# Kernel optimization log

Hardware: AMD Instinct MI355X
Metric: run time of the kernel (lower is better)

Reference implementation:

```python
import jax, jax.numpy as jnp
import numpy as np

EMBED_DIM = 1024
HIDDEN = 4 * EMBED_DIM
BATCH, SEQ = 4, 4096
EPS = 1e-5


def setup_inputs() -> dict:
    key = jax.random.key(0)
    k1, k2, k3 = jax.random.split(key, 3)
    x = jax.random.normal(k1, (BATCH, SEQ, EMBED_DIM), dtype=jnp.float32)
    # Kaiming-ish init scale for linear weights
    w1 = jax.random.normal(k2, (HIDDEN, EMBED_DIM), dtype=jnp.float32) * (1.0 / np.sqrt(EMBED_DIM))
    w2 = jax.random.normal(k3, (EMBED_DIM, HIDDEN), dtype=jnp.float32) * (1.0 / np.sqrt(HIDDEN))
    return {"x": x, "w1": w1, "w2": w2}


def _quant_weight(w):
    # BitNet-b1.58 absmean ternary quantization: clip(round(w/s), -1, 1) * s
    s = jnp.clip(jnp.mean(jnp.abs(w)), EPS, None)
    wq = jnp.clip(jnp.round(w / s), -1.0, 1.0) * s
    # straight-through estimator
    return w + jax.lax.stop_gradient(wq - w)


def _quant_act(x):
    # int8 per-token absmax quantization of activations
    scale = 127.0 / jnp.clip(jnp.max(jnp.abs(x), axis=-1, keepdims=True), EPS, None)
    xq = jnp.clip(jnp.round(x * scale), -128.0, 127.0) / scale
    return x + jax.lax.stop_gradient(xq - x)


def _bitlinear(x, w):
    # x: [..., in], w: [out, in] -> [..., out]
    return jnp.einsum('bsi,oi->bso', _quant_act(x), _quant_weight(w))


def reference(x, w1, w2):
    h = jax.nn.gelu(_bitlinear(x, w1), approximate=False)  # nn.GELU default = exact erf
    return _bitlinear(h, w2)  # dropout is identity in eval / p=0
```

## Files before the change

### kernel.cpp

```cpp
#include <hip/hip_runtime.h>
#include <hip/hip_bf16.h>
#include <cstdint>
#include <cmath>

typedef int intx4 __attribute__((ext_vector_type(4)));
typedef short shortx8 __attribute__((ext_vector_type(8)));

#define EPSQ 1e-5f

__device__ __forceinline__ void async16(const void* g, void* l) {
  __builtin_amdgcn_global_load_lds(
      (const __attribute__((address_space(1))) unsigned int*)(uintptr_t)g,
      (__attribute__((address_space(3))) unsigned int*)(unsigned int)(uintptr_t)l,
      16, 0, 0);
}

__device__ __forceinline__ int q8(float v, float scale, float lo, float hi) {
  return (int)fminf(fmaxf(rintf(v * scale), lo), hi);
}

__device__ __forceinline__ float fast_gelu(float y) {
  const float t = y * 0.70710678118654752f;
  const float x = fabsf(t);
  const float u = __builtin_amdgcn_rcpf(__builtin_fmaf(0.3275911f, x, 1.0f));
  float p = __builtin_fmaf(1.061405429f, u, -1.453152027f);
  p = __builtin_fmaf(p, u, 1.421413741f);
  p = __builtin_fmaf(p, u, -0.284496736f);
  p = __builtin_fmaf(p, u, 0.254829592f);
  p = p * u;
  const float e = __expf(-x * x);
  const float erf_abs = __builtin_fmaf(-p, e, 1.0f);
  const float erf_t = copysignf(erf_abs, t);
  return 0.5f * y * (1.0f + erf_t);
}

__global__ void k_init(float* rowmax, double* sums) {
  int i = blockIdx.x * 256 + threadIdx.x;
  if (i < 16384) rowmax[i] = 0.0f;
  if (i < 2) sums[i] = 0.0;
}

__global__ __launch_bounds__(256) void k_absmean2(const float* __restrict__ W1,
                                                  const float* __restrict__ W2,
                                                  double* __restrict__ sums) {
  __shared__ double wsum[4];
  const int tid = threadIdx.x;
  const int which = blockIdx.x >> 11;
  const float* __restrict__ W = which ? W2 : W1;
  const size_t base = ((size_t)(blockIdx.x & 2047) * 256 + tid) * 8;
  float4 a = *(const float4*)(W + base);
  float4 b = *(const float4*)(W + base + 4);
  float s = fabsf(a.x) + fabsf(a.y) + fabsf(a.z) + fabsf(a.w) +
            fabsf(b.x) + fabsf(b.y) + fabsf(b.z) + fabsf(b.w);
  double d = (double)s;
#pragma unroll
  for (int i = 1; i < 64; i <<= 1) d += __shfl_xor(d, i);
  const int lane = tid & 63, wave = tid >> 6;
  if (lane == 0) wsum[wave] = d;
  __syncthreads();
  if (tid == 0) atomicAdd(sums + which, wsum[0] + wsum[1] + wsum[2] + wsum[3]);
}

__global__ __launch_bounds__(256) void k_quantw2(const float* __restrict__ W1,
                                                 const float* __restrict__ W2,
                                                 signed char* __restrict__ W1Q,
                                                 signed char* __restrict__ W2Q,
                                                 const double* __restrict__ sums) {
  const int which = blockIdx.x >> 11;
  const float* __restrict__ W = which ? W2 : W1;
  signed char* __restrict__ WQ = which ? W2Q : W1Q;
  const float s = fmaxf((float)(sums[which] * (1.0 / 4194304.0)), EPSQ);
  const float inv_s = 1.0f / s;
  const size_t base = ((size_t)(blockIdx.x & 2047) * 256 + threadIdx.x) * 8;
  float4 a = *(const float4*)(W + base);
  float4 b = *(const float4*)(W + base + 4);
  float v[8] = {a.x, a.y, a.z, a.w, b.x, b.y, b.z, b.w};
  unsigned int lo = 0, hi = 0;
#pragma unroll
  for (int j = 0; j < 4; ++j) {
    lo |= ((unsigned int)(q8(v[j], inv_s, -1.f, 1.f) & 0xff)) << (8 * j);
    hi |= ((unsigned int)(q8(v[4 + j], inv_s, -1.f, 1.f) & 0xff)) << (8 * j);
  }
  uint2 o; o.x = lo; o.y = hi;
  *(uint2*)(WQ + base) = o;
}

__global__ __launch_bounds__(256) void k_quantx(const float* __restrict__ X,
                                                signed char* __restrict__ XQ,
                                                float* __restrict__ dqx) {
  __shared__ float wmax[4];
  const int row = blockIdx.x, tid = threadIdx.x;
  const size_t base = (size_t)row * 1024 + tid * 4;
  float4 a = *(const float4*)(X + base);
  float m = fmaxf(fmaxf(fabsf(a.x), fabsf(a.y)), fmaxf(fabsf(a.z), fabsf(a.w)));
#pragma unroll
  for (int i = 1; i < 64; i <<= 1) m = fmaxf(m, __shfl_xor(m, i));
  const int lane = tid & 63, wave = tid >> 6;
  if (lane == 0) wmax[wave] = m;
  __syncthreads();
  m = fmaxf(fmaxf(wmax[0], wmax[1]), fmaxf(wmax[2], wmax[3]));
  m = fmaxf(m, EPSQ);
  const float scale = 127.f / m;
  if (tid == 0) dqx[row] = m * (1.f / 127.f);
  unsigned int p = ((unsigned int)(q8(a.x, scale, -128.f, 127.f) & 0xff)) |
                   ((unsigned int)(q8(a.y, scale, -128.f, 127.f) & 0xff) << 8) |
                   ((unsigned int)(q8(a.z, scale, -128.f, 127.f) & 0xff) << 16) |
                   ((unsigned int)(q8(a.w, scale, -128.f, 127.f) & 0xff) << 24);
  *(unsigned int*)(XQ + base) = p;
}

template <int KB>
__device__ __forceinline__ void gemm_mainloop256(const signed char* __restrict__ A,
                                                 const signed char* __restrict__ B,
                                                 int bm, int bn, int tid, char* lds,
                                                 intx4 (&acc)[8][4]) {
  const int wave = tid >> 6, lane = tid & 63;
  const int wm = wave >> 2, wn = wave & 3;
  const int kq = lane >> 4, lc = lane & 15;
  constexpr int NT = KB / 64;

  size_t goff[4];
  int ldsbase[4];
#pragma unroll
  for (int i = 0; i < 4; ++i) {
    const int n = i * 512 + tid;
    const int m = n & 1023;
    const int r = m >> 2, g = m & 3;
    const int gl = g ^ ((r >> 1) & 3);
    const int rowbase = ((i < 2) ? bm : bn) * 256 + r;
    goff[i] = (size_t)rowbase * KB + gl * 16;
    ldsbase[i] = (i * 512 + wave * 64) * 16;
  }

  int aoff[8], boff[4];
#pragma unroll
  for (int mi = 0; mi < 8; ++mi) {
    const int r = wm * 128 + mi * 16 + lc;
    aoff[mi] = r * 64 + ((kq ^ ((r >> 1) & 3)) << 4);
  }
#pragma unroll
  for (int ni = 0; ni < 4; ++ni) {
    const int r = wn * 64 + ni * 16 + lc;
    boff[ni] = 16384 + r * 64 + ((kq ^ ((r >> 1) & 3)) << 4);
  }

#pragma unroll
  for (int mi = 0; mi < 8; ++mi)
#pragma unroll
    for (int ni = 0; ni < 4; ++ni) {
      intx4 z = {0, 0, 0, 0};
      acc[mi][ni] = z;
    }

#pragma unroll
  for (int t = 0; t < 3; ++t) {
    char* lslot = lds + (t & 3) * 32768;
    const size_t k0 = (size_t)t * 64;
#pragma unroll
    for (int i = 0; i < 4; ++i)
      async16(((i < 2) ? A : B) + goff[i] + k0, lslot + ldsbase[i]);
  }

  for (int t = 0; t < NT; ++t) {
    if (t + 2 < NT)      asm volatile("s_waitcnt vmcnt(8)" ::: "memory");
    else if (t + 1 < NT) asm volatile("s_waitcnt vmcnt(4)" ::: "memory");
    else                 asm volatile("s_waitcnt vmcnt(0)" ::: "memory");
    __builtin_amdgcn_s_barrier();
    __builtin_amdgcn_sched_barrier(0);
    if (t + 3 < NT) {
      char* lslot = lds + ((t + 3) & 3) * 32768;
      const size_t k0 = (size_t)(t + 3) * 64;
#pragma unroll
      for (int i = 0; i < 4; ++i)
        async16(((i < 2) ? A : B) + goff[i] + k0, lslot + ldsbase[i]);
    }
    char* lslot = lds + (t & 3) * 32768;
    intx4 af[8], bf[4];
#pragma unroll
    for (int mi = 0; mi < 8; ++mi) af[mi] = *(const intx4*)(lslot + aoff[mi]);
#pragma unroll
    for (int ni = 0; ni < 4; ++ni) bf[ni] = *(const intx4*)(lslot + boff[ni]);
    __builtin_amdgcn_s_setprio(1);
#pragma unroll
    for (int mi = 0; mi < 8; ++mi)
#pragma unroll
      for (int ni = 0; ni < 4; ++ni)
        acc[mi][ni] =
            __builtin_amdgcn_mfma_i32_16x16x64_i8(af[mi], bf[ni], acc[mi][ni], 0, 0, 0);
    __builtin_amdgcn_s_setprio(0);
  }
}

__global__ __launch_bounds__(512, 2) void k_gemm1(const signed char* __restrict__ A,
                                                  const signed char* __restrict__ B,
                                                  const float* __restrict__ dqx,
                                                  const double* __restrict__ sums,
                                                  short* __restrict__ HS,
                                                  float* __restrict__ mblk,
                                                  float* __restrict__ rowmax) {
  __shared__ __attribute__((aligned(16))) char lds[131072];
  const int tid = threadIdx.x;
  const int bm = blockIdx.x, bn = blockIdx.y;

  intx4 acc[8][4];
  gemm_mainloop256<1024>(A, B, bm, bn, tid, lds, acc);

  const int wave = tid >> 6, lane = tid & 63;
  const int wm = wave >> 2, wn = wave & 3;
  const int kq = lane >> 4, lc = lane & 15;
  const float s1 = fmaxf((float)(sums[0] * (1.0 / 4194304.0)), EPSQ);

  __syncthreads();
  float* smax = (float*)lds;
  if (tid < 256) smax[tid] = 0.0f;
  __syncthreads();

#pragma unroll
  for (int mi = 0; mi < 8; ++mi) {
#pragma unroll
    for (int r = 0; r < 4; ++r) {
      const int lrow = wm * 128 + mi * 16 + kq * 4 + r;
      const int crow = bm * 256 + lrow;
      const float f = s1 * dqx[crow];
      float mx = 0.f;
#pragma unroll
      for (int ni = 0; ni < 4; ++ni) {
        float y = (float)acc[mi][ni][r] * f;
        float h = fast_gelu(y);
        acc[mi][ni][r] = (int)__float_as_uint(h);
        mx = fmaxf(mx, fabsf(h));
      }
#pragma unroll
      for (int s = 1; s < 16; s <<= 1) mx = fmaxf(mx, __shfl_xor(mx, s));
      if (lc == 0) atomicMax((unsigned int*)&smax[lrow], __float_as_uint(mx));
    }
  }
  __syncthreads();
  if (tid < 256) {
    mblk[(size_t)(bm * 256 + tid) * 16 + bn] = smax[tid];
    atomicMax((unsigned int*)&rowmax[bm * 256 + tid], __float_as_uint(smax[tid]));
  }

#pragma unroll
  for (int mi = 0; mi < 8; ++mi) {
#pragma unroll
    for (int r = 0; r < 4; ++r) {
      const int lrow = wm * 128 + mi * 16 + kq * 4 + r;
      const int crow = bm * 256 + lrow;
      const float sc = 32767.0f / fmaxf(smax[lrow], 1e-30f);
#pragma unroll
      for (int ni = 0; ni < 4; ++ni) {
        const int gcol = bn * 256 + wn * 64 + ni * 16 + lc;
        float h = __uint_as_float((unsigned int)acc[mi][ni][r]);
        int v = (int)fminf(fmaxf(rintf(h * sc), -32767.f), 32767.f);
        HS[(size_t)crow * 4096 + gcol] = (short)v;
      }
    }
  }
}

__global__ __launch_bounds__(256) void k_quanth(const short* __restrict__ HS,
                                                const float* __restrict__ mblk,
                                                const float* __restrict__ rowmax,
                                                signed char* __restrict__ HQ) {
  const size_t gid = (size_t)blockIdx.x * 256 + threadIdx.x;
  const size_t base = gid * 8;
  const int row = (int)(base >> 12);
  const int blk = (int)((base >> 8) & 15);
  const float m = fmaxf(rowmax[row], EPSQ);
  const float fb = mblk[(size_t)row * 16 + blk] * (127.0f / 32767.0f) / m;
  shortx8 s = *(const shortx8*)(HS + base);
  unsigned int lo = 0, hi = 0;
#pragma unroll
  for (int j = 0; j < 4; ++j) {
    lo |= ((unsigned int)(q8((float)s[j], fb, -128.f, 127.f) & 0xff)) << (8 * j);
    hi |= ((unsigned int)(q8((float)s[4 + j], fb, -128.f, 127.f) & 0xff)) << (8 * j);
  }
  uint2 o; o.x = lo; o.y = hi;
  *(uint2*)(HQ + base) = o;
}

__global__ __launch_bounds__(512, 2) void k_gemm2(const signed char* __restrict__ A,
                                                  const signed char* __restrict__ B,
                                                  const float* __restrict__ rowmax,
                                                  const double* __restrict__ sums,
                                                  float* __restrict__ OUT) {
  __shared__ __attribute__((aligned(16))) char lds[131072];
  const int tid = threadIdx.x;
  const int bm = blockIdx.x, bn = blockIdx.y;

  intx4 acc[8][4];
  gemm_mainloop256<4096>(A, B, bm, bn, tid, lds, acc);

  const int wave = tid >> 6, lane = tid & 63;
  const int wm = wave >> 2, wn = wave & 3;
  const int kq = lane >> 4, lc = lane & 15;
  const float s2 = fmaxf((float)(sums[0] * (1.0 / 4194304.0)), EPSQ);
#pragma unroll
  for (int mi = 0; mi < 8; ++mi) {
#pragma unroll
    for (int r = 0; r < 4; ++r) {
      const int crow = bm * 256 + wm * 128 + mi * 16 + kq * 4 + r;
      const float dqh = fmaxf(rowmax[crow], EPSQ) * (1.f / 127.f);
      const float f = s2 * dqh;
#pragma unroll
      for (int ni = 0; ni < 4; ++ni) {
        const int gcol = bn * 256 + wn * 64 + ni * 16 + lc;
        OUT[(size_t)crow * 1024 + gcol] = (float)acc[mi][ni][r] * f;
      }
    }
  }
}

extern "C" void kernel_launch(void* const* d_in, const int* in_sizes, int n_in,
                              void* d_out, int out_size, void* d_ws, size_t ws_size,
                              hipStream_t stream) {
  const float* X  = (const float*)d_in[0];
  const float* W1 = (const float*)d_in[1];
  const float* W2 = (const float*)d_in[2];
  float* OUT = (float*)d_out;

  char* ws = (char*)d_ws;
  signed char* W1Q = (signed char*)(ws);
  signed char* W2Q = (signed char*)(ws + (4u << 20));
  float* DQX       = (float*)(ws + (8u << 20));
  float* ROWMAX    = (float*)(ws + (8u << 20) + 65536);
  double* SUMS     = (double*)(ws + (8u << 20) + 131072);
  float* MBLK      = (float*)(ws + (9u << 20));
  signed char* HQ  = (signed char*)(ws + (10u << 20));
  const size_t fixed = 74u << 20;
  short* HS = (short*)(ws + fixed);

  signed char* XQ = (signed char*)((char*)d_out + 50331648ull);

  int R = 256;
  const int cands[7] = {16384, 8192, 4096, 2048, 1024, 512, 256};
  for (int i = 0; i < 7; ++i) {
    if (fixed + (size_t)cands[i] * 8192ull <= ws_size) { R = cands[i]; break; }
  }

  hipLaunchKernelGGL(k_init, dim3(64), dim3(256), 0, stream, ROWMAX, SUMS);
  hipLaunchKernelGGL(k_absmean2, dim3(4096), dim3(256), 0, stream, W1, W2, SUMS);
  hipLaunchKernelGGL(k_quantw2, dim3(4096), dim3(256), 0, stream, W1, W2, W1Q, W2Q, SUMS);
  hipLaunchKernelGGL(k_quantx, dim3(16384), dim3(256), 0, stream, X, XQ, DQX);

  const int nchunk = 16384 / R;
  for (int c = 0; c < nchunk; ++c) {
    const int row0 = c * R;
    hipLaunchKernelGGL(k_gemm1, dim3(R / 256, 16), dim3(512), 0, stream,
                       XQ + (size_t)row0 * 1024, W1Q, DQX + row0, SUMS,
                       HS, MBLK + (size_t)row0 * 16, ROWMAX + row0);
    hipLaunchKernelGGL(k_quanth, dim3(R * 2), dim3(256), 0, stream,
                       HS, MBLK + (size_t)row0 * 16, ROWMAX + row0,
                       HQ + (size_t)row0 * 4096);
  }
  hipLaunchKernelGGL(k_gemm2, dim3(64, 4), dim3(512), 0, stream,
                     HQ, W2Q, ROWMAX, SUMS + 1, OUT);
}
```

Before: 418.5 us.

## Restructure GEMM mainloop to double-buffered K=128 stages, swizzle tiles, pack intermediate

The shared GEMM mainloop moves from a 4-slot K=64 async pipeline to a 2-slot K=128 double buffer with an XOR-swizzled LDS layout. The next-stage global loads are spread across four sub-phases that each end in a barrier, so loads overlap MFMA work. Both GEMMs now use a 1D grid with a block-index swizzle to improve L2 reuse. The gemm1 epilogue writes the int16 intermediate as vectorized 4-row packed words using v_cvt_pknorm_i16_f32, and k_quanth reads that packed layout, which adds layout complexity and slightly different rounding.

```diff
diff --git a/kernel.cpp b/kernel.cpp
--- a/kernel.cpp
+++ b/kernel.cpp
@@ -4,7 +4,6 @@
 #include <cmath>
 
 typedef int intx4 __attribute__((ext_vector_type(4)));
-typedef short shortx8 __attribute__((ext_vector_type(8)));
 
 #define EPSQ 1e-5f
 
@@ -17,6 +16,12 @@
 
 __device__ __forceinline__ int q8(float v, float scale, float lo, float hi) {
   return (int)fminf(fmaxf(rintf(v * scale), lo), hi);
+}
+
+__device__ __forceinline__ unsigned int pknorm_i16(float a, float b) {
+  unsigned int r;
+  asm("v_cvt_pknorm_i16_f32 %0, %1, %2" : "=v"(r) : "v"(a), "v"(b));
+  return r;
 }
 
 __device__ __forceinline__ float fast_gelu(float y) {
@@ -117,32 +122,20 @@
   const int wave = tid >> 6, lane = tid & 63;
   const int wm = wave >> 2, wn = wave & 3;
   const int kq = lane >> 4, lc = lane & 15;
-  constexpr int NT = KB / 64;
-
-  size_t goff[4];
-  int ldsbase[4];
-#pragma unroll
-  for (int i = 0; i < 4; ++i) {
-    const int n = i * 512 + tid;
-    const int m = n & 1023;
-    const int r = m >> 2, g = m & 3;
-    const int gl = g ^ ((r >> 1) & 3);
-    const int rowbase = ((i < 2) ? bm : bn) * 256 + r;
-    goff[i] = (size_t)rowbase * KB + gl * 16;
-    ldsbase[i] = (i * 512 + wave * 64) * 16;
-  }
-
-  int aoff[8], boff[4];
-#pragma unroll
-  for (int mi = 0; mi < 8; ++mi) {
-    const int r = wm * 128 + mi * 16 + lc;
-    aoff[mi] = r * 64 + ((kq ^ ((r >> 1) & 3)) << 4);
-  }
-#pragma unroll
-  for (int ni = 0; ni < 4; ++ni) {
-    const int r = wn * 64 + ni * 16 + lc;
-    boff[ni] = 16384 + r * 64 + ((kq ^ ((r >> 1) & 3)) << 4);
-  }
+  constexpr int NS = KB / 128;
+
+  const int rr = tid >> 3;
+  const int gs16 = (((tid & 7) ^ (rr & 7)) << 4);
+  unsigned int goff[8];
+#pragma unroll
+  for (int j = 0; j < 8; ++j) {
+    const int rowbase = ((j < 4) ? bm : bn) * 256 + (j & 3) * 64 + rr;
+    goff[j] = (unsigned int)rowbase * (unsigned int)KB + gs16;
+  }
+
+  const int fsw = ((kq ^ (lc & 7)) << 4);
+  const int abase = (wm * 128 + lc) * 128 + fsw;
+  const int bbase = 32768 + (wn * 64 + lc) * 128 + fsw;
 
 #pragma unroll
   for (int mi = 0; mi < 8; ++mi)
@@ -153,41 +146,66 @@
     }
 
 #pragma unroll
-  for (int t = 0; t < 3; ++t) {
-    char* lslot = lds + (t & 3) * 32768;
-    const size_t k0 = (size_t)t * 64;
-#pragma unroll
-    for (int i = 0; i < 4; ++i)
-      async16(((i < 2) ? A : B) + goff[i] + k0, lslot + ldsbase[i]);
-  }
-
-  for (int t = 0; t < NT; ++t) {
-    if (t + 2 < NT)      asm volatile("s_waitcnt vmcnt(8)" ::: "memory");
-    else if (t + 1 < NT) asm volatile("s_waitcnt vmcnt(4)" ::: "memory");
-    else                 asm volatile("s_waitcnt vmcnt(0)" ::: "memory");
-    __builtin_amdgcn_s_barrier();
-    __builtin_amdgcn_sched_barrier(0);
-    if (t + 3 < NT) {
-      char* lslot = lds + ((t + 3) & 3) * 32768;
-      const size_t k0 = (size_t)(t + 3) * 64;
-#pragma unroll
-      for (int i = 0; i < 4; ++i)
-        async16(((i < 2) ? A : B) + goff[i] + k0, lslot + ldsbase[i]);
+  for (int j = 0; j < 8; ++j)
+    async16(((j < 4) ? A : B) + (size_t)goff[j],
+            lds + j * 8192 + wave * 1024);
+  asm volatile("s_waitcnt vmcnt(0)" ::: "memory");
+  __builtin_amdgcn_s_barrier();
+  __builtin_amdgcn_sched_barrier(0);
+
+  for (int t = 0; t < NS; ++t) {
+    char* buf = lds + ((t & 1) << 16);
+    char* nbuf = lds + (((t + 1) & 1) << 16);
+    const size_t k0n = (size_t)(t + 1) * 128;
+    const bool more = (t + 1 < NS);
+    intx4 bf[4][2];
+#pragma unroll
+    for (int p = 0; p < 4; ++p) {
+      intx4 af[2][2];
+#pragma unroll
+      for (int h = 0; h < 2; ++h) {
+        const int o = abase + (2 * p + h) * 2048;
+        af[h][0] = *(const intx4*)(buf + o);
+        af[h][1] = *(const intx4*)(buf + (o ^ 64));
+      }
+      if (p == 0) {
+#pragma unroll
+        for (int ni = 0; ni < 4; ++ni) {
+          const int o = bbase + ni * 2048;
+          bf[ni][0] = *(const intx4*)(buf + o);
+          bf[ni][1] = *(const intx4*)(buf + (o ^ 64));
+        }
+      }
+      if (more) {
+        if (p == 0) {
+          async16(A + (size_t)goff[0] + k0n, nbuf + 0 * 8192 + wave * 1024);
+          async16(A + (size_t)goff[1] + k0n, nbuf + 1 * 8192 + wave * 1024);
+          async16(A + (size_t)goff[2] + k0n, nbuf + 2 * 8192 + wave * 1024);
+        } else if (p == 1) {
+          async16(A + (size_t)goff[3] + k0n, nbuf + 3 * 8192 + wave * 1024);
+          async16(B + (size_t)goff[4] + k0n, nbuf + 4 * 8192 + wave * 1024);
+          async16(B + (size_t)goff[5] + k0n, nbuf + 5 * 8192 + wave * 1024);
+        } else if (p == 2) {
+          async16(B + (size_t)goff[6] + k0n, nbuf + 6 * 8192 + wave * 1024);
+          async16(B + (size_t)goff[7] + k0n, nbuf + 7 * 8192 + wave * 1024);
+        }
+      }
+      __builtin_amdgcn_s_barrier();
+      __builtin_amdgcn_sched_barrier(0);
+      __builtin_amdgcn_s_setprio(1);
+#pragma unroll
+      for (int ks = 0; ks < 2; ++ks)
+#pragma unroll
+        for (int h = 0; h < 2; ++h)
+#pragma unroll
+          for (int ni = 0; ni < 4; ++ni)
+            acc[2 * p + h][ni] = __builtin_amdgcn_mfma_i32_16x16x64_i8(
+                af[h][ks], bf[ni][ks], acc[2 * p + h][ni], 0, 0, 0);
+      __builtin_amdgcn_s_setprio(0);
+      __builtin_amdgcn_sched_barrier(0);
+      if (p == 3 && more) asm volatile("s_waitcnt vmcnt(0)" ::: "memory");
+      __builtin_amdgcn_s_barrier();
     }
-    char* lslot = lds + (t & 3) * 32768;
-    intx4 af[8], bf[4];
-#pragma unroll
-    for (int mi = 0; mi < 8; ++mi) af[mi] = *(const intx4*)(lslot + aoff[mi]);
-#pragma unroll
-    for (int ni = 0; ni < 4; ++ni) bf[ni] = *(const intx4*)(lslot + boff[ni]);
-    __builtin_amdgcn_s_setprio(1);
-#pragma unroll
-    for (int mi = 0; mi < 8; ++mi)
-#pragma unroll
-      for (int ni = 0; ni < 4; ++ni)
-        acc[mi][ni] =
-            __builtin_amdgcn_mfma_i32_16x16x64_i8(af[mi], bf[ni], acc[mi][ni], 0, 0, 0);
-    __builtin_amdgcn_s_setprio(0);
   }
 }
 
@@ -195,12 +213,15 @@
                                                   const signed char* __restrict__ B,
                                                   const float* __restrict__ dqx,
                                                   const double* __restrict__ sums,
-                                                  short* __restrict__ HS,
+                                                  short* __restrict__ HSP,
                                                   float* __restrict__ mblk,
                                                   float* __restrict__ rowmax) {
   __shared__ __attribute__((aligned(16))) char lds[131072];
   const int tid = threadIdx.x;
-  const int bm = blockIdx.x, bn = blockIdx.y;
+  const int q = gridDim.x >> 3;
+  const int fid = blockIdx.x;
+  const int swz = (fid & 7) * q + (fid >> 3);
+  const int bm = swz >> 4, bn = swz & 15;
 
   intx4 acc[8][4];
   gemm_mainloop256<1024>(A, B, bm, bn, tid, lds, acc);
@@ -243,41 +264,67 @@
 
 #pragma unroll
   for (int mi = 0; mi < 8; ++mi) {
-#pragma unroll
-    for (int r = 0; r < 4; ++r) {
-      const int lrow = wm * 128 + mi * 16 + kq * 4 + r;
-      const int crow = bm * 256 + lrow;
-      const float sc = 32767.0f / fmaxf(smax[lrow], 1e-30f);
-#pragma unroll
-      for (int ni = 0; ni < 4; ++ni) {
-        const int gcol = bn * 256 + wn * 64 + ni * 16 + lc;
-        float h = __uint_as_float((unsigned int)acc[mi][ni][r]);
-        int v = (int)fminf(fmaxf(rintf(h * sc), -32767.f), 32767.f);
-        HS[(size_t)crow * 4096 + gcol] = (short)v;
-      }
+    const int lrow0 = wm * 128 + mi * 16 + kq * 4;
+    const int qr = (bm * 256 + lrow0) >> 2;
+    float inv[4];
+#pragma unroll
+    for (int r = 0; r < 4; ++r)
+      inv[r] = __builtin_amdgcn_rcpf(fmaxf(smax[lrow0 + r], 1e-30f));
+#pragma unroll
+    for (int ni = 0; ni < 4; ++ni) {
+      const int gcol = bn * 256 + wn * 64 + ni * 16 + lc;
+      const float h0 = __uint_as_float((unsigned int)acc[mi][ni][0]) * inv[0];
+      const float h1 = __uint_as_float((unsigned int)acc[mi][ni][1]) * inv[1];
+      const float h2 = __uint_as_float((unsigned int)acc[mi][ni][2]) * inv[2];
+      const float h3 = __uint_as_float((unsigned int)acc[mi][ni][3]) * inv[3];
+      uint2 o;
+      o.x = pknorm_i16(h0, h1);
+      o.y = pknorm_i16(h2, h3);
+      *(uint2*)(HSP + ((size_t)qr * 4096 + gcol) * 4) = o;
     }
   }
 }
 
-__global__ __launch_bounds__(256) void k_quanth(const short* __restrict__ HS,
+__global__ __launch_bounds__(256) void k_quanth(const short* __restrict__ HSP,
                                                 const float* __restrict__ mblk,
                                                 const float* __restrict__ rowmax,
                                                 signed char* __restrict__ HQ) {
-  const size_t gid = (size_t)blockIdx.x * 256 + threadIdx.x;
-  const size_t base = gid * 8;
-  const int row = (int)(base >> 12);
-  const int blk = (int)((base >> 8) & 15);
-  const float m = fmaxf(rowmax[row], EPSQ);
-  const float fb = mblk[(size_t)row * 16 + blk] * (127.0f / 32767.0f) / m;
-  shortx8 s = *(const shortx8*)(HS + base);
-  unsigned int lo = 0, hi = 0;
-#pragma unroll
-  for (int j = 0; j < 4; ++j) {
-    lo |= ((unsigned int)(q8((float)s[j], fb, -128.f, 127.f) & 0xff)) << (8 * j);
-    hi |= ((unsigned int)(q8((float)s[4 + j], fb, -128.f, 127.f) & 0xff)) << (8 * j);
-  }
-  uint2 o; o.x = lo; o.y = hi;
-  *(uint2*)(HQ + base) = o;
+  const int gid = blockIdx.x * 256 + threadIdx.x;
+  const int qr = gid >> 8;
+  const int cg = gid & 255;
+  const int c0 = cg * 16;
+  const int blk = c0 >> 8;
+  const int row0 = qr * 4;
+  float fb[4];
+#pragma unroll
+  for (int r = 0; r < 4; ++r) {
+    const float m = fmaxf(rowmax[row0 + r], EPSQ);
+    fb[r] = mblk[(size_t)(row0 + r) * 16 + blk] * (127.0f / 32767.0f) / m;
+  }
+  const uint4* src = (const uint4*)(HSP + ((size_t)qr * 4096 + c0) * 4);
+  uint4 L[8];
+#pragma unroll
+  for (int j = 0; j < 8; ++j) L[j] = src[j];
+
+  unsigned int out[4][4] = {};
+#pragma unroll
+  for (int j = 0; j < 16; ++j) {
+    const unsigned int u01 = (j & 1) ? L[j >> 1].z : L[j >> 1].x;
+    const unsigned int u23 = (j & 1) ? L[j >> 1].w : L[j >> 1].y;
+    const float s0 = (float)(short)(u01 & 0xffff);
+    const float s1 = (float)(short)(u01 >> 16);
+    const float s2 = (float)(short)(u23 & 0xffff);
+    const float s3 = (float)(short)(u23 >> 16);
+    out[0][j >> 2] |= ((unsigned int)(q8(s0, fb[0], -128.f, 127.f) & 0xff)) << (8 * (j & 3));
+    out[1][j >> 2] |= ((unsigned int)(q8(s1, fb[1], -128.f, 127.f) & 0xff)) << (8 * (j & 3));
+    out[2][j >> 2] |= ((unsigned int)(q8(s2, fb[2], -128.f, 127.f) & 0xff)) << (8 * (j & 3));
+    out[3][j >> 2] |= ((unsigned int)(q8(s3, fb[3], -128.f, 127.f) & 0xff)) << (8 * (j & 3));
+  }
+#pragma unroll
+  for (int r = 0; r < 4; ++r) {
+    uint4 o; o.x = out[r][0]; o.y = out[r][1]; o.z = out[r][2]; o.w = out[r][3];
+    *(uint4*)(HQ + (size_t)(row0 + r) * 4096 + c0) = o;
+  }
 }
 
 __global__ __launch_bounds__(512, 2) void k_gemm2(const signed char* __restrict__ A,
@@ -287,7 +334,10 @@
                                                   float* __restrict__ OUT) {
   __shared__ __attribute__((aligned(16))) char lds[131072];
   const int tid = threadIdx.x;
-  const int bm = blockIdx.x, bn = blockIdx.y;
+  const int q = gridDim.x >> 3;
+  const int fid = blockIdx.x;
+  const int swz = (fid & 7) * q + (fid >> 3);
+  const int bm = swz >> 2, bn = swz & 3;
 
   intx4 acc[8][4];
   gemm_mainloop256<4096>(A, B, bm, bn, tid, lds, acc);
@@ -329,7 +379,7 @@
   float* MBLK      = (float*)(ws + (9u << 20));
   signed char* HQ  = (signed char*)(ws + (10u << 20));
   const size_t fixed = 74u << 20;
-  short* HS = (short*)(ws + fixed);
+  short* HSP = (short*)(ws + fixed);
 
   signed char* XQ = (signed char*)((char*)d_out + 50331648ull);
 
@@ -347,13 +397,13 @@
   const int nchunk = 16384 / R;
   for (int c = 0; c < nchunk; ++c) {
     const int row0 = c * R;
-    hipLaunchKernelGGL(k_gemm1, dim3(R / 256, 16), dim3(512), 0, stream,
+    hipLaunchKernelGGL(k_gemm1, dim3((R / 256) * 16), dim3(512), 0, stream,
                        XQ + (size_t)row0 * 1024, W1Q, DQX + row0, SUMS,
-                       HS, MBLK + (size_t)row0 * 16, ROWMAX + row0);
-    hipLaunchKernelGGL(k_quanth, dim3(R * 2), dim3(256), 0, stream,
-                       HS, MBLK + (size_t)row0 * 16, ROWMAX + row0,
+                       HSP, MBLK + (size_t)row0 * 16, ROWMAX + row0);
+    hipLaunchKernelGGL(k_quanth, dim3(R / 4), dim3(256), 0, stream,
+                       HSP, MBLK + (size_t)row0 * 16, ROWMAX + row0,
                        HQ + (size_t)row0 * 4096);
   }
-  hipLaunchKernelGGL(k_gemm2, dim3(64, 4), dim3(512), 0, stream,
+  hipLaunchKernelGGL(k_gemm2, dim3(256), dim3(512), 0, stream,
                      HQ, W2Q, ROWMAX, SUMS + 1, OUT);
 }
```

Result: faster. 408.0 us (-2.5%).
